# Kernel tuning notes

Measured on AMD Instinct MI355X. Metric: run time of the kernel, lower is better.

The kernel has to match this reference:

```python
import jax, jax.numpy as jnp
import numpy as np
from jax import lax

B, T, D_IN, D_OUT = 1, 24000, 598, 3
UNITS = [100, 100, 100]
EPS = 0.001


def _lstm(x, W, U, b):
    # x: [B,T,D]; W: [D,4U]; U: [U,4U]; b: [4U]. Keras gate order i,f,g,o.
    units = U.shape[0]
    xW = jnp.einsum('btd,dk->btk', x, W) + b  # precompute input projections

    def step(carry, xw_t):
        h, c = carry
        z = xw_t + h @ U
        i, f, g, o = jnp.split(z, 4, axis=-1)
        c = jax.nn.sigmoid(f) * c + jax.nn.sigmoid(i) * jnp.tanh(g)
        h = jax.nn.sigmoid(o) * jnp.tanh(c)
        return (h, c), h

    h0 = jnp.zeros((x.shape[0], units), x.dtype)
    (_, _), hs = lax.scan(step, (h0, h0), jnp.swapaxes(xW, 0, 1))
    return jnp.swapaxes(hs, 0, 1)  # [B,T,U]


def _bn(x, gamma, beta, mean, var):
    # inference-mode batch norm over last axis
    return (x - mean) * lax.rsqrt(var + EPS) * gamma + beta


def setup_inputs() -> dict:
    key = jax.random.key(0)
    ks = jax.random.split(key, 16)
    out = {"x": jax.random.normal(ks[0], (B, T, D_IN), jnp.float32)}
    d_prev = D_IN
    ki = 1
    for l, u in enumerate(UNITS, start=1):
        out[f"W{l}"] = jax.random.normal(ks[ki], (d_prev, 4 * u), jnp.float32) * (2.0 / d_prev) ** 0.5; ki += 1
        out[f"U{l}"] = jax.random.normal(ks[ki], (u, 4 * u), jnp.float32) * (1.0 / u) ** 0.5; ki += 1
        out[f"b{l}"] = jnp.zeros((4 * u,), jnp.float32)
        out[f"g{l}"] = jnp.ones((u,), jnp.float32)
        out[f"be{l}"] = jnp.zeros((u,), jnp.float32)
        out[f"m{l}"] = jnp.zeros((u,), jnp.float32)
        out[f"v{l}"] = jnp.ones((u,), jnp.float32)
        d_prev = u
    out["Wd"] = jax.random.normal(ks[ki], (d_prev, D_OUT), jnp.float32) * (2.0 / d_prev) ** 0.5
    out["bd"] = jnp.zeros((D_OUT,), jnp.float32)
    return out


def reference(x, W1, U1, b1, g1, be1, m1, v1,
              W2, U2, b2, g2, be2, m2, v2,
              W3, U3, b3, g3, be3, m3, v3, Wd, bd):
    h = x
    params = [(W1, U1, b1, g1, be1, m1, v1),
              (W2, U2, b2, g2, be2, m2, v2),
              (W3, U3, b3, g3, be3, m3, v3)]
    for (W, U, b, g, be, m, v) in params:
        h = _lstm(h, W, U, b)
        h = _bn(h, g, be, m, v)
    return jax.nn.softmax(h @ Wd + bd, axis=-1)
```

## Files before the change

### kernel.cpp

```cpp
#include <hip/hip_runtime.h>

#define T_STEPS 24000
#define DIN 598
#define NU 100
#define NG 400
#define KHALF 52
#define KPAD 104
#define CHUNK 120
#define NCHUNK 200
#define RING 8
#define RN (RING * CHUNK)

#define BARRIER_LDS() asm volatile("s_waitcnt lgkmcnt(0)\n\ts_barrier" ::: "memory")

__device__ __forceinline__ void wg_wait_ge(int* flag, int target) {
    if (threadIdx.x == 0) {
        while (__hip_atomic_load(flag, __ATOMIC_RELAXED, __HIP_MEMORY_SCOPE_AGENT) < target)
            __builtin_amdgcn_s_sleep(2);
    }
    __syncthreads();
    __builtin_amdgcn_fence(__ATOMIC_ACQUIRE, "agent");
}
__device__ __forceinline__ void wg_publish(int* a, int va, int* b, int vb) {
    __syncthreads();
    if (threadIdx.x == 0) {
        if (a) __hip_atomic_store(a, va, __ATOMIC_RELEASE, __HIP_MEMORY_SCOPE_AGENT);
        if (b) __hip_atomic_store(b, vb, __ATOMIC_RELEASE, __HIP_MEMORY_SCOPE_AGENT);
    }
}

__device__ __forceinline__ float sigmoid_(float x) {
    return 1.f / (1.f + __expf(-x));
}
__device__ __forceinline__ float tanh_(float x) {
    float e = __expf(2.f * x);
    return 1.f - 2.f / (e + 1.f);
}

__global__ __launch_bounds__(256) void gemm_bias_kernel(
    const float* __restrict__ A, const float* __restrict__ B,
    const float* __restrict__ bias, float* __restrict__ C,
    int M, int N, int K)
{
    __shared__ float As[16][65];
    __shared__ float Bs[16][65];
    const int tid = threadIdx.x;
    const int tx = tid & 15;
    const int ty = tid >> 4;
    const int bm = blockIdx.y * 64;
    const int bn = blockIdx.x * 64;
    float acc[4][4] = {};

    for (int k0 = 0; k0 < K; k0 += 16) {
        #pragma unroll
        for (int p = 0; p < 4; ++p) {
            int e = tid + p * 256;
            int r = e >> 4, cc = e & 15;
            int m = bm + r, k = k0 + cc;
            float v = (m < M && k < K) ? A[(long)m * K + k] : 0.f;
            As[cc][r] = v;
        }
        #pragma unroll
        for (int p = 0; p < 4; ++p) {
            int e = tid + p * 256;
            int r = e >> 6, cc = e & 63;
            int k = k0 + r, n = bn + cc;
            float v = (k < K && n < N) ? B[(long)k * N + n] : 0.f;
            Bs[r][cc] = v;
        }
        __syncthreads();
        #pragma unroll
        for (int kk = 0; kk < 16; ++kk) {
            float a[4], b[4];
            #pragma unroll
            for (int i = 0; i < 4; ++i) a[i] = As[kk][ty * 4 + i];
            #pragma unroll
            for (int j = 0; j < 4; ++j) b[j] = Bs[kk][tx * 4 + j];
            #pragma unroll
            for (int i = 0; i < 4; ++i)
                #pragma unroll
                for (int j = 0; j < 4; ++j)
                    acc[i][j] += a[i] * b[j];
        }
        __syncthreads();
    }
    #pragma unroll
    for (int i = 0; i < 4; ++i) {
        int m = bm + ty * 4 + i;
        if (m >= M) continue;
        #pragma unroll
        for (int j = 0; j < 4; ++j) {
            int n = bn + tx * 4 + j;
            if (n < N) {
                int pn = (n % 100) * 4 + (n / 100);
                C[(long)m * N + pn] = acc[i][j] + bias[n];
            }
        }
    }
}

__device__ void rec_role(
    const float* __restrict__ xz, int xz_ring,
    const float* __restrict__ U,
    float* __restrict__ hout, int h_ring,
    int* flag_up, int* done_self, int* done_down, int* flag_self,
    float* lds)
{
    float* hb0 = lds;
    float* hb1 = lds + KPAD;
    const int tid = threadIdx.x;
    const bool active = tid < 2 * NU;
    const int u = tid >> 1;
    const int s = tid & 1;

    float4 uf[KHALF];
    if (active) {
        const int k0 = KHALF * s;
        #pragma unroll
        for (int i = 0; i < KHALF; ++i) {
            int k = k0 + i;
            uf[i] = (k < NU)
                ? make_float4(U[(long)k * NG + u],       U[(long)k * NG + NU + u],
                              U[(long)k * NG + 2 * NU + u], U[(long)k * NG + 3 * NU + u])
                : make_float4(0.f, 0.f, 0.f, 0.f);
        }
    }
    if (tid < KPAD) { hb0[tid] = 0.f; hb1[tid] = 0.f; }
    float c_state = 0.f;
    float2 xw0 = make_float2(0.f, 0.f), xw1 = xw0;
    __syncthreads();

    auto step = [&](const float* hrd, float* hwr, int t) {
        if (active) {
            const float4* h4 = (const float4*)(hrd + KHALF * s);
            float ax = 0.f, ay = 0.f, az = 0.f, aw = 0.f;
            #pragma unroll
            for (int q = 0; q < 13; ++q) {
                float4 hv = h4[q];
                float hh[4] = {hv.x, hv.y, hv.z, hv.w};
                #pragma unroll
                for (int j = 0; j < 4; ++j) {
                    float4 uv = uf[4 * q + j];
                    ax += uv.x * hh[j];
                    ay += uv.y * hh[j];
                    az += uv.z * hh[j];
                    aw += uv.w * hh[j];
                }
            }
            if (s == 0) { ax += xw0.x; ay += xw0.y; }
            else        { az += xw0.x; aw += xw0.y; }
            xw0 = xw1;
            int tp = t + 2;
            if (tp < T_STEPS) {
                long rr = xz_ring ? (long)(tp % RN) : (long)tp;
                xw1 = *(const float2*)&xz[rr * NG + 4 * u + 2 * s];
            }
            ax += __shfl_xor(ax, 1);
            ay += __shfl_xor(ay, 1);
            az += __shfl_xor(az, 1);
            aw += __shfl_xor(aw, 1);
            float iv = sigmoid_(ax);
            float fv = sigmoid_(ay);
            float gv = tanh_(az);
            float ov = sigmoid_(aw);
            c_state = fv * c_state + iv * gv;
            float h = ov * tanh_(c_state);
            if (s == 0) {
                hwr[u] = h;
                long orow = h_ring ? (long)(t % RN) : (long)t;
                hout[orow * NU + u] = h;
            }
        }
        BARRIER_LDS();
    };

    for (int c = 0; c < NCHUNK; ++c) {
        if (flag_up) {
            int tgt = c + 2; if (tgt > NCHUNK) tgt = NCHUNK;
            wg_wait_ge(flag_up, tgt);
        }
        if (done_down && c >= RING) wg_wait_ge(done_down, c - RING + 1);
        if (c == 0 && active) {
            xw0 = *(const float2*)&xz[4 * u + 2 * s];
            xw1 = *(const float2*)&xz[NG + 4 * u + 2 * s];
        }
        const int t0 = c * CHUNK;
        for (int tt = 0; tt < CHUNK; tt += 2) {
            step(hb0, hb1, t0 + tt);
            step(hb1, hb0, t0 + tt + 1);
        }
        wg_publish(done_self, c + 1, flag_self, c + 1);
    }
}

__device__ void proj_role(
    const float* __restrict__ hin,
    const float* __restrict__ W,
    const float* __restrict__ bias,
    const float* __restrict__ g, const float* __restrict__ be,
    const float* __restrict__ m, const float* __restrict__ v,
    float* __restrict__ xzout,
    int* flag_up, int* done_self, int* done_down, int* flag_self,
    float* lds)
{
    const int tid = threadIdx.x;
    const bool active = tid < 2 * NU;
    const int u = tid >> 1;
    const int s = tid & 1;

    float4 wf[KHALF];
    float bx = 0.f, by = 0.f;
    if (active) {
        const int k0 = KHALF * s;
        float pbx = 0.f, pby = 0.f, pbz = 0.f, pbw = 0.f;
        #pragma unroll
        for (int i = 0; i < KHALF; ++i) {
            int k = k0 + i;
            if (k < NU) {
                float sc = g[k] * rsqrtf(v[k] + 1e-3f);
                float sh = be[k] - m[k] * sc;
                float w0 = W[(long)k * NG + u];
                float w1 = W[(long)k * NG + NU + u];
                float w2 = W[(long)k * NG + 2 * NU + u];
                float w3 = W[(long)k * NG + 3 * NU + u];
                wf[i] = make_float4(sc * w0, sc * w1, sc * w2, sc * w3);
                pbx += sh * w0; pby += sh * w1; pbz += sh * w2; pbw += sh * w3;
            } else {
                wf[i] = make_float4(0.f, 0.f, 0.f, 0.f);
            }
        }
        pbx += __shfl_xor(pbx, 1); pby += __shfl_xor(pby, 1);
        pbz += __shfl_xor(pbz, 1); pbw += __shfl_xor(pbw, 1);
        if (s == 0) { bx = bias[u]          + pbx; by = bias[NU + u]     + pby; }
        else        { bx = bias[2 * NU + u] + pbz; by = bias[3 * NU + u] + pbw; }
    }

    for (int c = 0; c < NCHUNK; ++c) {
        wg_wait_ge(flag_up, c + 1);
        if (c >= RING) wg_wait_ge(done_down, c - RING + 1);
        const float* src = hin + (size_t)(c % RING) * CHUNK * NU;
        for (int idx = tid; idx < CHUNK * KPAD; idx += 256) {
            int r = idx / KPAD, k = idx - r * KPAD;
            lds[idx] = (k < NU) ? src[r * NU + k] : 0.f;
        }
        wg_publish(done_self, c + 1, (int*)0, 0);
        if (active) {
            float* ob = xzout + (size_t)(c % RING) * CHUNK * NG;
            for (int r = 0; r < CHUNK; ++r) {
                const float4* h4 = (const float4*)(lds + r * KPAD + KHALF * s);
                float ax = 0.f, ay = 0.f, az = 0.f, aw = 0.f;
                #pragma unroll
                for (int q = 0; q < 13; ++q) {
                    float4 hv = h4[q];
                    float hh[4] = {hv.x, hv.y, hv.z, hv.w};
                    #pragma unroll
                    for (int j = 0; j < 4; ++j) {
                        float4 wv = wf[4 * q + j];
                        ax += wv.x * hh[j];
                        ay += wv.y * hh[j];
                        az += wv.z * hh[j];
                        aw += wv.w * hh[j];
                    }
                }
                ax += __shfl_xor(ax, 1);
                ay += __shfl_xor(ay, 1);
                az += __shfl_xor(az, 1);
                aw += __shfl_xor(aw, 1);
                float2 o2 = (s == 0) ? make_float2(ax + bx, ay + by)
                                     : make_float2(az + bx, aw + by);
                *(float2*)&ob[(long)r * NG + 4 * u + 2 * s] = o2;
            }
        }
        wg_publish(flag_self, c + 1, (int*)0, 0);
    }
}

__global__ __launch_bounds__(256, 1) void lstm_pipe_kernel(
    const float* xw1, const float* U1,
    const float* U2, const float* W2, const float* b2,
    const float* U3, const float* W3, const float* b3,
    const float* g1, const float* be1, const float* m1, const float* v1,
    const float* g2, const float* be2, const float* m2, const float* v2,
    float* h1r, float* h2r, float* xz2r, float* xz3r, float* h3,
    int* f)
{
    extern __shared__ float smem[];
    int* f_h1  = f +   0;
    int* d_p2  = f +  32;
    int* f_xz2 = f +  64;
    int* d_r2  = f +  96;
    int* f_h2  = f + 128;
    int* d_p3  = f + 160;
    int* f_xz3 = f + 192;
    int* d_r3  = f + 224;

    switch (blockIdx.x) {
    case 0: rec_role(xw1, 0, U1, h1r, 1, (int*)0, (int*)0, d_p2, f_h1, smem); break;
    case 1: proj_role(h1r, W2, b2, g1, be1, m1, v1, xz2r, f_h1, d_p2, d_r2, f_xz2, smem); break;
    case 2: rec_role(xz2r, 1, U2, h2r, 1, f_xz2, d_r2, d_p3, f_h2, smem); break;
    case 3: proj_role(h2r, W3, b3, g2, be2, m2, v2, xz3r, f_h2, d_p3, d_r3, f_xz3, smem); break;
    case 4: rec_role(xz3r, 1, U3, h3, 0, f_xz3, d_r3, (int*)0, (int*)0, smem); break;
    }
}

__global__ __launch_bounds__(256) void dense_softmax_kernel(
    const float* __restrict__ H,
    const float* __restrict__ Wd,
    const float* __restrict__ bd,
    const float* __restrict__ g3, const float* __restrict__ be3,
    const float* __restrict__ m3, const float* __restrict__ v3,
    float* __restrict__ out, int T)
{
    __shared__ float w[300];
    __shared__ float b[3];
    const int tid = threadIdx.x;
    for (int i = tid; i < 300; i += 256) {
        int k = i / 3;
        float sc = g3[k] * rsqrtf(v3[k] + 1e-3f);
        w[i] = Wd[i] * sc;
    }
    if (tid < 3) {
        float acc = bd[tid];
        for (int k = 0; k < NU; ++k) {
            float sc = g3[k] * rsqrtf(v3[k] + 1e-3f);
            float sh = be3[k] - m3[k] * sc;
            acc += sh * Wd[3 * k + tid];
        }
        b[tid] = acc;
    }
    __syncthreads();

    int row = blockIdx.x * blockDim.x + tid;
    if (row >= T) return;
    const float* h = H + (long)row * NU;
    float s0 = b[0], s1 = b[1], s2 = b[2];
    #pragma unroll 4
    for (int k = 0; k < NU; ++k) {
        float hv = h[k];
        s0 += hv * w[3 * k + 0];
        s1 += hv * w[3 * k + 1];
        s2 += hv * w[3 * k + 2];
    }
    float mx = fmaxf(s0, fmaxf(s1, s2));
    float e0 = __expf(s0 - mx), e1 = __expf(s1 - mx), e2 = __expf(s2 - mx);
    float inv = 1.f / (e0 + e1 + e2);
    out[(long)row * 3 + 0] = e0 * inv;
    out[(long)row * 3 + 1] = e1 * inv;
    out[(long)row * 3 + 2] = e2 * inv;
}

extern "C" void kernel_launch(void* const* d_in, const int* in_sizes, int n_in,
                              void* d_out, int out_size, void* d_ws, size_t ws_size,
                              hipStream_t stream)
{
    const float* x   = (const float*)d_in[0];
    const float* W1  = (const float*)d_in[1];
    const float* U1  = (const float*)d_in[2];
    const float* b1  = (const float*)d_in[3];
    const float* ga1 = (const float*)d_in[4];
    const float* be1 = (const float*)d_in[5];
    const float* mu1 = (const float*)d_in[6];
    const float* va1 = (const float*)d_in[7];
    const float* W2  = (const float*)d_in[8];
    const float* U2  = (const float*)d_in[9];
    const float* b2  = (const float*)d_in[10];
    const float* ga2 = (const float*)d_in[11];
    const float* be2 = (const float*)d_in[12];
    const float* mu2 = (const float*)d_in[13];
    const float* va2 = (const float*)d_in[14];
    const float* W3  = (const float*)d_in[15];
    const float* U3  = (const float*)d_in[16];
    const float* b3  = (const float*)d_in[17];
    const float* ga3 = (const float*)d_in[18];
    const float* be3 = (const float*)d_in[19];
    const float* mu3 = (const float*)d_in[20];
    const float* va3 = (const float*)d_in[21];
    const float* Wd  = (const float*)d_in[22];
    const float* bd  = (const float*)d_in[23];

    float* xw1  = (float*)d_ws;
    float* h3   = xw1  + (size_t)T_STEPS * NG;
    float* h1r  = h3   + (size_t)T_STEPS * NU;
    float* h2r  = h1r  + (size_t)RN * NU;
    float* xz2r = h2r  + (size_t)RN * NU;
    float* xz3r = xz2r + (size_t)RN * NG;
    int*   flags = (int*)(xz3r + (size_t)RN * NG);
    float* out = (float*)d_out;

    dim3 blk(256);
    dim3 grd((NG + 63) / 64, (T_STEPS + 63) / 64);

    gemm_bias_kernel<<<grd, blk, 0, stream>>>(x, W1, b1, xw1, T_STEPS, NG, DIN);
    hipMemsetAsync(flags, 0, 512 * sizeof(int), stream);
    lstm_pipe_kernel<<<5, 256, CHUNK * KPAD * sizeof(float), stream>>>(
        xw1, U1, U2, W2, b2, U3, W3, b3,
        ga1, be1, mu1, va1, ga2, be2, mu2, va2,
        h1r, h2r, xz2r, xz3r, h3, flags);
    dense_softmax_kernel<<<(T_STEPS + 255) / 256, 256, 0, stream>>>(
        h3, Wd, bd, ga3, be3, mu3, va3, out, T_STEPS);
}
```

Measured before the change: 20.73 ms.

## Store recurrent hidden states transposed in float4 batches and double the chunk size

```diff
diff --git a/kernel.cpp b/kernel.cpp
--- a/kernel.cpp
+++ b/kernel.cpp
@@ -6,9 +6,9 @@
 #define NG 400
 #define KHALF 52
 #define KPAD 104
-#define CHUNK 120
-#define NCHUNK 200
-#define RING 8
+#define CHUNK 240
+#define NCHUNK 100
+#define RING 4
 #define RN (RING * CHUNK)
 
 #define BARRIER_LDS() asm volatile("s_waitcnt lgkmcnt(0)\n\ts_barrier" ::: "memory")
@@ -102,7 +102,7 @@
 __device__ void rec_role(
     const float* __restrict__ xz, int xz_ring,
     const float* __restrict__ U,
-    float* __restrict__ hout, int h_ring,
+    float* __restrict__ hout, long h_stride, int h_ring,
     int* flag_up, int* done_self, int* done_down, int* flag_self,
     float* lds)
 {
@@ -128,6 +128,7 @@
     if (tid < KPAD) { hb0[tid] = 0.f; hb1[tid] = 0.f; }
     float c_state = 0.f;
     float2 xw0 = make_float2(0.f, 0.f), xw1 = xw0;
+    float4 hbatch = make_float4(0.f, 0.f, 0.f, 0.f);
     __syncthreads();
 
     auto step = [&](const float* hrd, float* hwr, int t) {
@@ -167,8 +168,15 @@
             float h = ov * tanh_(c_state);
             if (s == 0) {
                 hwr[u] = h;
-                long orow = h_ring ? (long)(t % RN) : (long)t;
-                hout[orow * NU + u] = h;
+                int ph = t & 3;
+                if      (ph == 0) hbatch.x = h;
+                else if (ph == 1) hbatch.y = h;
+                else if (ph == 2) hbatch.z = h;
+                else {
+                    hbatch.w = h;
+                    long tb = h_ring ? (long)((t - 3) % RN) : (long)(t - 3);
+                    *(float4*)&hout[(long)u * h_stride + tb] = hbatch;
+                }
             }
         }
         BARRIER_LDS();
@@ -238,10 +246,12 @@
     for (int c = 0; c < NCHUNK; ++c) {
         wg_wait_ge(flag_up, c + 1);
         if (c >= RING) wg_wait_ge(done_down, c - RING + 1);
-        const float* src = hin + (size_t)(c % RING) * CHUNK * NU;
-        for (int idx = tid; idx < CHUNK * KPAD; idx += 256) {
-            int r = idx / KPAD, k = idx - r * KPAD;
-            lds[idx] = (k < NU) ? src[r * NU + k] : 0.f;
+        {
+            const int tbase = (c % RING) * CHUNK;
+            for (int idx = tid; idx < KPAD * CHUNK; idx += 256) {
+                int k = idx / CHUNK, r = idx - k * CHUNK;
+                lds[r * KPAD + k] = (k < NU) ? hin[(long)k * RN + tbase + r] : 0.f;
+            }
         }
         wg_publish(done_self, c + 1, (int*)0, 0);
         if (active) {
@@ -295,11 +305,11 @@
     int* d_r3  = f + 224;
 
     switch (blockIdx.x) {
-    case 0: rec_role(xw1, 0, U1, h1r, 1, (int*)0, (int*)0, d_p2, f_h1, smem); break;
+    case 0: rec_role(xw1, 0, U1, h1r, RN, 1, (int*)0, (int*)0, d_p2, f_h1, smem); break;
     case 1: proj_role(h1r, W2, b2, g1, be1, m1, v1, xz2r, f_h1, d_p2, d_r2, f_xz2, smem); break;
-    case 2: rec_role(xz2r, 1, U2, h2r, 1, f_xz2, d_r2, d_p3, f_h2, smem); break;
+    case 2: rec_role(xz2r, 1, U2, h2r, RN, 1, f_xz2, d_r2, d_p3, f_h2, smem); break;
     case 3: proj_role(h2r, W3, b3, g2, be2, m2, v2, xz3r, f_h2, d_p3, d_r3, f_xz3, smem); break;
-    case 4: rec_role(xz3r, 1, U3, h3, 0, f_xz3, d_r3, (int*)0, (int*)0, smem); break;
+    case 4: rec_role(xz3r, 1, U3, h3, T_STEPS, 0, f_xz3, d_r3, (int*)0, (int*)0, smem); break;
     }
 }
 
@@ -332,11 +342,10 @@
 
     int row = blockIdx.x * blockDim.x + tid;
     if (row >= T) return;
-    const float* h = H + (long)row * NU;
     float s0 = b[0], s1 = b[1], s2 = b[2];
     #pragma unroll 4
     for (int k = 0; k < NU; ++k) {
-        float hv = h[k];
+        float hv = H[(long)k * T + row];
         s0 += hv * w[3 * k + 0];
         s1 += hv * w[3 * k + 1];
         s2 += hv * w[3 * k + 2];
```

New measurement: 18.90 ms. 1.1x faster.
